# Optimization experiments

Measured on AMD Instinct MI355X. Metric: run time of the kernel, lower is better.

Reference implementation:

```python
import jax, jax.numpy as jnp
import numpy as np

B, T, C, H = 4, 2048, 768, 12
D = C // H  # head dim = 64

def setup_inputs() -> dict:
    key = jax.random.key(0)
    k1, k2, k3 = jax.random.split(key, 3)
    x = jax.random.normal(k1, (B, T, C), dtype=jnp.float32)
    W_attn = jax.random.normal(k2, (C, 3 * C), dtype=jnp.float32) * 0.02
    b_attn = jnp.zeros((3 * C,), dtype=jnp.float32)
    W_proj = jax.random.normal(k3, (C, C), dtype=jnp.float32) * 0.02
    b_proj = jnp.zeros((C,), dtype=jnp.float32)
    return {"x": x, "W_attn": W_attn, "b_attn": b_attn, "W_proj": W_proj, "b_proj": b_proj}

def reference(x, W_attn, b_attn, W_proj, b_proj):
    Bx, Tx, Cx = x.shape
    qkv = x @ W_attn + b_attn                      # [B,T,3C]
    q, k, v = jnp.split(qkv, 3, axis=2)
    q = q.reshape(Bx, Tx, H, D).swapaxes(1, 2)     # [B,H,T,D]
    k = k.reshape(Bx, Tx, H, D).swapaxes(1, 2)
    v = v.reshape(Bx, Tx, H, D).swapaxes(1, 2)
    att = jnp.einsum('bhqd,bhkd->bhqk', q, k) / jnp.sqrt(jnp.float32(D))
    mask = jnp.tril(jnp.ones((Tx, Tx), dtype=bool))
    att = jnp.where(mask, att, -jnp.inf)
    att = jax.nn.softmax(att, axis=-1)
    y = jnp.einsum('bhqk,bhkd->bhqd', att, v)      # [B,H,T,D]
    y = y.swapaxes(1, 2).reshape(Bx, Tx, Cx)
    return y @ W_proj + b_proj
```

## Files before the change

### kernel.cpp

```cpp
#include <hip/hip_runtime.h>
#include <hip/hip_bf16.h>

#define BATCH 4
#define TSEQ  2048
#define CDIM  768
#define HNUM  12
#define DHEAD 64
#define NQKV  (3*CDIM)
#define BTOT  (BATCH*TSEQ)
#define BH    (BATCH*HNUM)

typedef unsigned short u16;
typedef __attribute__((ext_vector_type(8))) __bf16 bf16x8;
typedef __attribute__((ext_vector_type(4))) float f32x4;

#define MFMA16(a,b,c) __builtin_amdgcn_mfma_f32_16x16x32_bf16((a),(b),(c),0,0,0)

__device__ __forceinline__ u16 f2b(float f) {
    union { float f; unsigned u; } v; v.f = f;
    unsigned u = v.u;
    unsigned r = (u + 0x7fffu + ((u >> 16) & 1u)) >> 16;
    return (u16)r;
}

__device__ __forceinline__ unsigned cvtpk(float lo, float hi) {
    unsigned r;
    asm("v_cvt_pk_bf16_f32 %0, %1, %2" : "=v"(r) : "v"(lo), "v"(hi));
    return r;
}

__device__ __forceinline__ float fexp2(float x) {
    float r;
    asm("v_exp_f32 %0, %1" : "=v"(r) : "v"(x));
    return r;
}

__device__ __forceinline__ void gload_lds(const void* g, void* l) {
    __builtin_amdgcn_global_load_lds(
        (const __attribute__((address_space(1))) void*)g,
        (__attribute__((address_space(3))) void*)l, 16, 0, 0);
}

#define CAST_BLKS (BTOT * CDIM / 4 / 256)
#define TA_BLKS   ((NQKV / 32) * (CDIM / 32))
#define TP_BLKS   ((CDIM / 32) * (CDIM / 32))
__global__ __launch_bounds__(256) void prep(
        const float* __restrict__ x, u16* __restrict__ xb,
        const float* __restrict__ Wa, const float* __restrict__ Wp,
        u16* __restrict__ WaT, u16* __restrict__ WpT) {
    __shared__ float tile[32][33];
    const int bx = blockIdx.x, tid = threadIdx.x;
    if (bx < CAST_BLKS) {
        int i = bx * 256 + tid;
        float4 a = reinterpret_cast<const float4*>(x)[i];
        ushort4 o;
        o.x = f2b(a.x); o.y = f2b(a.y); o.z = f2b(a.z); o.w = f2b(a.w);
        reinterpret_cast<ushort4*>(xb)[i] = o;
        return;
    }
    int bz = bx - CAST_BLKS;
    const float* in; u16* out; int Cc;
    int nxa = NQKV / 32;
    int cx, ry;
    if (bz < TA_BLKS) { in = Wa; out = WaT; Cc = NQKV; cx = bz % nxa; ry = bz / nxa; }
    else { bz -= TA_BLKS; in = Wp; out = WpT; Cc = CDIM; cx = bz % (CDIM/32); ry = bz / (CDIM/32); }
    int c0 = cx * 32, r0 = ry * 32;
    int tx = tid & 31, ty = tid >> 5;
    #pragma unroll
    for (int i = 0; i < 32; i += 8)
        tile[ty + i][tx] = in[(size_t)(r0 + ty + i) * Cc + c0 + tx];
    __syncthreads();
    #pragma unroll
    for (int i = 0; i < 32; i += 8)
        out[(size_t)(c0 + ty + i) * CDIM + r0 + tx] = f2b(tile[tx][ty + i]);
}

template<int NX>
__global__ __launch_bounds__(512) void gemm_qkv(
        const u16* __restrict__ A, const u16* __restrict__ Bt,
        const float* __restrict__ bias,
        u16* __restrict__ qb, u16* __restrict__ kb, u16* __restrict__ vtb,
        int K) {
    __shared__ u16 sA[2][256 * 32];
    __shared__ u16 sB[2][128 * 32];
    const int tid = threadIdx.x;
    const int lane = tid & 63;
    const int w = tid >> 6;
    const int wr = w >> 1, wc = w & 1;
    const int g = lane >> 4, lq = lane & 15;
    const int cpx = gridDim.x >> 3;
    const int wg = ((int)blockIdx.x & 7) * cpx + ((int)blockIdx.x >> 3);
    const int bx = wg % NX, by = wg / NX;
    const int m0 = by * 256, n0 = bx * 128;

    f32x4 acc[4][4] = {};

    auto stage = [&](int buf, int kt) {
        #pragma unroll
        for (int i = 0; i < 2; ++i) {
            int c = i * 512 + tid;
            int r = c >> 2, s = c & 3;
            int l = s ^ ((r >> 1) & 3);
            gload_lds(A + (size_t)(m0 + r) * K + kt * 32 + l * 8, &sA[buf][c * 8]);
        }
        {
            int c = tid;
            int r = c >> 2, s = c & 3;
            int l = s ^ ((r >> 1) & 3);
            gload_lds(Bt + (size_t)(n0 + r) * K + kt * 32 + l * 8, &sB[buf][c * 8]);
        }
    };

    const int KT = K / 32;
    stage(0, 0);
    __syncthreads();
    for (int kt = 0; kt < KT; ++kt) {
        if (kt + 1 < KT) stage((kt + 1) & 1, kt + 1);
        const u16* cA = sA[kt & 1];
        const u16* cB = sB[kt & 1];
        bf16x8 af[4], bfr[4];
        #pragma unroll
        for (int m = 0; m < 4; ++m) {
            int r = wr * 64 + m * 16 + lq;
            af[m] = *(const bf16x8*)&cA[r * 32 + ((g ^ ((r >> 1) & 3)) << 3)];
        }
        #pragma unroll
        for (int n = 0; n < 4; ++n) {
            int r = wc * 64 + n * 16 + lq;
            bfr[n] = *(const bf16x8*)&cB[r * 32 + ((g ^ ((r >> 1) & 3)) << 3)];
        }
        #pragma unroll
        for (int m = 0; m < 4; ++m)
            #pragma unroll
            for (int n = 0; n < 4; ++n)
                acc[m][n] = MFMA16(bfr[n], af[m], acc[m][n]);
        __syncthreads();
    }

    const int which = n0 / CDIM;
    #pragma unroll
    for (int m = 0; m < 4; ++m) {
        const int rg = m0 + wr * 64 + m * 16 + lq;
        const int b = rg >> 11, t = rg & (TSEQ - 1);
        #pragma unroll
        for (int n = 0; n < 4; ++n) {
            const int cg = n0 + wc * 64 + n * 16 + (g << 2);
            const int c  = cg - which * CDIM;
            const int h  = c >> 6, d = c & 63;
            const size_t bh = (size_t)(b * HNUM + h);
            const float4 bv = *(const float4*)&bias[cg];
            const float v0 = acc[m][n][0] + bv.x;
            const float v1 = acc[m][n][1] + bv.y;
            const float v2 = acc[m][n][2] + bv.z;
            const float v3 = acc[m][n][3] + bv.w;
            if (which == 0) {
                const float s = 0.1803368801111243f;
                ushort4 pv;
                pv.x = f2b(v0 * s); pv.y = f2b(v1 * s);
                pv.z = f2b(v2 * s); pv.w = f2b(v3 * s);
                *(ushort4*)&qb[(bh * TSEQ + t) * DHEAD + d] = pv;
            } else if (which == 1) {
                ushort4 pv;
                pv.x = f2b(v0); pv.y = f2b(v1); pv.z = f2b(v2); pv.w = f2b(v3);
                *(ushort4*)&kb[(bh * TSEQ + t) * DHEAD + d] = pv;
            } else {
                vtb[(bh * DHEAD + d + 0) * TSEQ + t] = f2b(v0);
                vtb[(bh * DHEAD + d + 1) * TSEQ + t] = f2b(v1);
                vtb[(bh * DHEAD + d + 2) * TSEQ + t] = f2b(v2);
                vtb[(bh * DHEAD + d + 3) * TSEQ + t] = f2b(v3);
            }
        }
    }
}

template<int NX>
__global__ __launch_bounds__(256) void gemm_out(
        const u16* __restrict__ A, const u16* __restrict__ Bt,
        const float* __restrict__ bias, float* __restrict__ outf, int K) {
    __shared__ u16 sA[2][64 * 32];
    __shared__ u16 sB[2][128 * 32];
    const int tid = threadIdx.x;
    const int lane = tid & 63;
    const int w = tid >> 6;
    const int wr = w >> 1, wc = w & 1;
    const int g = lane >> 4, lq = lane & 15;
    const int cpx = gridDim.x >> 3;
    const int wg = ((int)blockIdx.x & 7) * cpx + ((int)blockIdx.x >> 3);
    const int bx = wg % NX, by = wg / NX;
    const int m0 = by * 64, n0 = bx * 128;

    f32x4 acc[2][4] = {};

    auto stage = [&](int buf, int kt) {
        {
            int c = tid;
            int r = c >> 2, s = c & 3;
            int l = s ^ ((r >> 1) & 3);
            gload_lds(A + (size_t)(m0 + r) * K + kt * 32 + l * 8, &sA[buf][c * 8]);
        }
        #pragma unroll
        for (int i = 0; i < 2; ++i) {
            int c = i * 256 + tid;
            int r = c >> 2, s = c & 3;
            int l = s ^ ((r >> 1) & 3);
            gload_lds(Bt + (size_t)(n0 + r) * K + kt * 32 + l * 8, &sB[buf][c * 8]);
        }
    };

    const int KT = K / 32;
    stage(0, 0);
    __syncthreads();
    for (int kt = 0; kt < KT; ++kt) {
        if (kt + 1 < KT) stage((kt + 1) & 1, kt + 1);
        const u16* cA = sA[kt & 1];
        const u16* cB = sB[kt & 1];
        bf16x8 af[2], bfr[4];
        #pragma unroll
        for (int m = 0; m < 2; ++m) {
            int r = wr * 32 + m * 16 + lq;
            af[m] = *(const bf16x8*)&cA[r * 32 + ((g ^ ((r >> 1) & 3)) << 3)];
        }
        #pragma unroll
        for (int n = 0; n < 4; ++n) {
            int r = wc * 64 + n * 16 + lq;
            bfr[n] = *(const bf16x8*)&cB[r * 32 + ((g ^ ((r >> 1) & 3)) << 3)];
        }
        #pragma unroll
        for (int m = 0; m < 2; ++m)
            #pragma unroll
            for (int n = 0; n < 4; ++n)
                acc[m][n] = MFMA16(bfr[n], af[m], acc[m][n]);
        __syncthreads();
    }

    #pragma unroll
    for (int m = 0; m < 2; ++m) {
        const int rg = m0 + wr * 32 + m * 16 + lq;
        #pragma unroll
        for (int n = 0; n < 4; ++n) {
            const int cg = n0 + wc * 64 + n * 16 + (g << 2);
            const float4 bv = *(const float4*)&bias[cg];
            float4 ov;
            ov.x = acc[m][n][0] + bv.x;
            ov.y = acc[m][n][1] + bv.y;
            ov.z = acc[m][n][2] + bv.z;
            ov.w = acc[m][n][3] + bv.w;
            *(float4*)&outf[(size_t)rg * CDIM + cg] = ov;
        }
    }
}

__global__ __launch_bounds__(256, 5) void attn_fwd(
        const u16* __restrict__ qb, const u16* __restrict__ kb,
        const u16* __restrict__ vtb, u16* __restrict__ yb) {
    __shared__ u16 sK[2][64 * 64];
    __shared__ u16 sVt[2][64 * 64];
    const int qt = 31 - (int)(blockIdx.x / BH);
    const int bh = blockIdx.x % BH;
    const int b = bh / HNUM, h = bh % HNUM;
    const int tid = threadIdx.x, lane = tid & 63, w = tid >> 6;
    const int g = lane >> 4, lq = lane & 15;
    const int qlo = qt * 64 + w * 16;
    const u16* qbase = qb  + (size_t)bh * TSEQ * DHEAD;
    const u16* kbase = kb  + (size_t)bh * TSEQ * DHEAD;
    const u16* vbase = vtb + (size_t)bh * DHEAD * TSEQ;

    bf16x8 qf[2];
    #pragma unroll
    for (int ks = 0; ks < 2; ++ks)
        qf[ks] = *(const bf16x8*)&qbase[(size_t)(qlo + lq) * DHEAD + ks * 32 + g * 8];

    union { unsigned u[4]; bf16x8 v; } ones;
    #pragma unroll
    for (int i = 0; i < 4; ++i) ones.u[i] = 0x3f803f80u;

    f32x4 o[4] = {};
    f32x4 ls = {};
    float mx = -__builtin_inff();

    auto STAGE = [&](int buf, int kt) {
        const int k0 = kt << 6;
        #pragma unroll
        for (int i = 0; i < 2; ++i) {
            int chunk = i * 256 + tid;
            int srow = chunk >> 3;
            int cb = ((chunk & 7) << 4) ^ ((srow & 7) << 4);
            gload_lds(kbase + (size_t)(k0 + srow) * DHEAD + (cb >> 1), &sK[buf][chunk * 8]);
            gload_lds(vbase + (size_t)srow * TSEQ + k0 + (cb >> 1),    &sVt[buf][chunk * 8]);
        }
    };

    const int nk = qt + 1;
    STAGE(0, 0);
    __syncthreads();
    for (int kt = 0; kt < nk; ++kt) {
        const int k0 = kt << 6;
        if (kt + 1 < nk) STAGE((kt + 1) & 1, kt + 1);
        const u16* cK = sK[kt & 1];
        const u16* cV = sVt[kt & 1];
        f32x4 s[4];
        #pragma unroll
        for (int n = 0; n < 4; ++n) s[n] = f32x4{0.f, 0.f, 0.f, 0.f};
        __builtin_amdgcn_s_setprio(1);
        #pragma unroll
        for (int n = 0; n < 4; ++n) {
            #pragma unroll
            for (int ks = 0; ks < 2; ++ks) {
                int r = n * 16 + lq;
                int lb = (r * 128 + (ks * 32 + g * 8) * 2) ^ ((r & 7) << 4);
                bf16x8 kf = *(const bf16x8*)((const char*)cK + lb);
                s[n] = MFMA16(kf, qf[ks], s[n]);
            }
        }
        __builtin_amdgcn_s_setprio(0);
        if (k0 + 63 > qlo) {
            const int qa = qlo + lq;
            #pragma unroll
            for (int n = 0; n < 4; ++n)
                #pragma unroll
                for (int j = 0; j < 4; ++j)
                    if (k0 + n * 16 + g * 4 + j > qa) s[n][j] = -__builtin_inff();
        }
        float t0 = fmaxf(fmaxf(s[0][0], s[0][1]), fmaxf(s[0][2], s[0][3]));
        float t1 = fmaxf(fmaxf(s[1][0], s[1][1]), fmaxf(s[1][2], s[1][3]));
        float t2 = fmaxf(fmaxf(s[2][0], s[2][1]), fmaxf(s[2][2], s[2][3]));
        float t3 = fmaxf(fmaxf(s[3][0], s[3][1]), fmaxf(s[3][2], s[3][3]));
        float tmax = fmaxf(fmaxf(t0, t1), fmaxf(t2, t3));
        tmax = fmaxf(tmax, __shfl_xor(tmax, 16));
        tmax = fmaxf(tmax, __shfl_xor(tmax, 32));
        if (__any(tmax > mx + 8.0f)) {
            float mnew = fmaxf(mx, tmax);
            float sc = fexp2(mx - mnew);
            mx = mnew;
            #pragma unroll
            for (int j = 0; j < 4; ++j) {
                float scj = __shfl(sc, (lane & 48) | ((g << 2) + j));
                ls[j] *= scj;
                #pragma unroll
                for (int n = 0; n < 4; ++n) o[n][j] *= scj;
            }
        }
        #pragma unroll
        for (int n = 0; n < 4; ++n)
            #pragma unroll
            for (int j = 0; j < 4; ++j)
                s[n][j] = fexp2(s[n][j] - mx);
        unsigned apk[4], bpk[4];
        #pragma unroll
        for (int n = 0; n < 4; ++n) {
            apk[n] = cvtpk(s[n][0], s[n][1]);
            bpk[n] = cvtpk(s[n][2], s[n][3]);
        }
        const int s0l = lq + ((lane & 16) << 1);
        const bool hi = (lane & 32) != 0;
        #pragma unroll
        for (int ks = 0; ks < 2; ++ks) {
            unsigned A0  = (unsigned)__shfl((int)apk[2 * ks],     s0l);
            unsigned B0  = (unsigned)__shfl((int)bpk[2 * ks],     s0l);
            unsigned A1  = (unsigned)__shfl((int)apk[2 * ks + 1], s0l);
            unsigned B1  = (unsigned)__shfl((int)bpk[2 * ks + 1], s0l);
            unsigned A0h = (unsigned)__shfl((int)apk[2 * ks],     s0l + 16);
            unsigned B0h = (unsigned)__shfl((int)bpk[2 * ks],     s0l + 16);
            unsigned A1h = (unsigned)__shfl((int)apk[2 * ks + 1], s0l + 16);
            unsigned B1h = (unsigned)__shfl((int)bpk[2 * ks + 1], s0l + 16);
            union { unsigned u[4]; bf16x8 v; } pa;
            pa.u[0] = hi ? A1  : A0;
            pa.u[1] = hi ? B1  : B0;
            pa.u[2] = hi ? A1h : A0h;
            pa.u[3] = hi ? B1h : B0h;
            __builtin_amdgcn_s_setprio(1);
            #pragma unroll
            for (int n = 0; n < 4; ++n) {
                int d = n * 16 + lq;
                int lb = (d * 128 + (ks * 32 + g * 8) * 2) ^ ((d & 7) << 4);
                bf16x8 vf = *(const bf16x8*)((const char*)cV + lb);
                o[n] = MFMA16(pa.v, vf, o[n]);
            }
            ls = MFMA16(pa.v, ones.v, ls);
            __builtin_amdgcn_s_setprio(0);
        }
        __syncthreads();
    }

    #pragma unroll
    for (int j = 0; j < 4; ++j) {
        float inv = 1.f / ls[j];
        const int t = qlo + g * 4 + j;
        #pragma unroll
        for (int n = 0; n < 4; ++n) {
            const int c = h * DHEAD + n * 16 + lq;
            yb[((size_t)b * TSEQ + t) * CDIM + c] = f2b(o[n][j] * inv);
        }
    }
}

extern "C" void kernel_launch(void* const* d_in, const int* in_sizes, int n_in,
                              void* d_out, int out_size, void* d_ws, size_t ws_size,
                              hipStream_t stream) {
    const float* x      = (const float*)d_in[0];
    const float* W_attn = (const float*)d_in[1];
    const float* b_attn = (const float*)d_in[2];
    const float* W_proj = (const float*)d_in[3];
    const float* b_proj = (const float*)d_in[4];
    float* out = (float*)d_out;

    u16* ws = (u16*)d_ws;
    u16* xb     = ws;
    u16* yb     = xb;
    u16* WattnT = xb     + (size_t)BTOT * CDIM;
    u16* WprojT = WattnT + (size_t)NQKV * CDIM;
    u16* qb     = WprojT + (size_t)CDIM * CDIM;
    u16* kb     = qb     + (size_t)BH * TSEQ * DHEAD;
    u16* vtb    = kb     + (size_t)BH * TSEQ * DHEAD;

    prep<<<dim3(CAST_BLKS + TA_BLKS + TP_BLKS), 256, 0, stream>>>(
        x, xb, W_attn, W_proj, WattnT, WprojT);

    gemm_qkv<NQKV / 128><<<dim3((NQKV / 128) * (BTOT / 256)), 512, 0, stream>>>(
        xb, WattnT, b_attn, qb, kb, vtb, CDIM);

    attn_fwd<<<dim3((TSEQ / 64) * BH), 256, 0, stream>>>(qb, kb, vtb, yb);

    gemm_out<CDIM / 128><<<dim3((CDIM / 128) * (BTOT / 64)), 256, 0, stream>>>(
        yb, WprojT, b_proj, out, CDIM);
}
```

Measured before the change: 140.9 us.

## Triple-buffer QKV GEMM with BK=64 and interleaved load/MFMA phases

Changes the QKV projection GEMM from a double-buffered K-step of 32 to a triple-buffered K-step of 64. Prefetch now runs two tiles ahead, with an explicit vmcnt wait in place of __syncthreads. Each iteration is split into four sub-phases that interleave global-to-LDS staging, LDS fragment loads, and MFMA bursts, with setprio raised around the MFMAs. The goal is to hide memory latency and cut loop overhead per K element. The costs are much more LDS per block (about 144KB), which can limit occupancy, plus many extra barriers.

```diff
diff --git a/kernel.cpp b/kernel.cpp
--- a/kernel.cpp
+++ b/kernel.cpp
@@ -81,8 +81,8 @@
         const float* __restrict__ bias,
         u16* __restrict__ qb, u16* __restrict__ kb, u16* __restrict__ vtb,
         int K) {
-    __shared__ u16 sA[2][256 * 32];
-    __shared__ u16 sB[2][128 * 32];
+    __shared__ u16 sA[3][256 * 64];
+    __shared__ u16 sB[3][128 * 64];
     const int tid = threadIdx.x;
     const int lane = tid & 63;
     const int w = tid >> 6;
@@ -95,46 +95,90 @@
 
     f32x4 acc[4][4] = {};
 
-    auto stage = [&](int buf, int kt) {
-        #pragma unroll
-        for (int i = 0; i < 2; ++i) {
-            int c = i * 512 + tid;
-            int r = c >> 2, s = c & 3;
-            int l = s ^ ((r >> 1) & 3);
-            gload_lds(A + (size_t)(m0 + r) * K + kt * 32 + l * 8, &sA[buf][c * 8]);
-        }
-        {
-            int c = tid;
-            int r = c >> 2, s = c & 3;
-            int l = s ^ ((r >> 1) & 3);
-            gload_lds(Bt + (size_t)(n0 + r) * K + kt * 32 + l * 8, &sB[buf][c * 8]);
-        }
+    auto STA = [&](int buf, int t, int i) {
+        int c = i * 512 + tid;
+        int r = c >> 3, ks = (c >> 2) & 1, s = c & 3;
+        int l = s ^ ((r >> 1) & 3);
+        gload_lds(A + (size_t)(m0 + r) * K + t * 64 + ks * 32 + l * 8,
+                  &sA[buf][c * 8]);
     };
-
-    const int KT = K / 32;
-    stage(0, 0);
-    __syncthreads();
-    for (int kt = 0; kt < KT; ++kt) {
-        if (kt + 1 < KT) stage((kt + 1) & 1, kt + 1);
-        const u16* cA = sA[kt & 1];
-        const u16* cB = sB[kt & 1];
-        bf16x8 af[4], bfr[4];
+    auto STB = [&](int buf, int t, int i) {
+        int c = i * 512 + tid;
+        int r = c >> 3, ks = (c >> 2) & 1, s = c & 3;
+        int l = s ^ ((r >> 1) & 3);
+        gload_lds(Bt + (size_t)(n0 + r) * K + t * 64 + ks * 32 + l * 8,
+                  &sB[buf][c * 8]);
+    };
+    auto STALL6 = [&](int buf, int t) {
+        STA(buf, t, 0); STA(buf, t, 1); STA(buf, t, 2); STA(buf, t, 3);
+        STB(buf, t, 0); STB(buf, t, 1);
+    };
+
+    const int KT = K / 64;
+    STALL6(0, 0);
+    STALL6(1, 1);
+    for (int t = 0; t < KT; ++t) {
+        if (t + 1 < KT) asm volatile("s_waitcnt vmcnt(6)" ::: "memory");
+        else            asm volatile("s_waitcnt vmcnt(0)" ::: "memory");
+        __builtin_amdgcn_s_barrier();
+        const u16* cA = sA[t % 3];
+        const u16* cB = sB[t % 3];
+        const int nb = (t + 2) % 3;
+        const bool pre = (t + 2) < KT;
+
+        bf16x8 af[4], bf0, bf1;
+        #define LDA(m, ks) (*(const bf16x8*)&cA[(wr*64 + (m)*16 + lq) * 64 + (ks)*32 \
+                              + ((g ^ (((wr*64 + (m)*16 + lq) >> 1) & 3)) << 3)])
+        #define LDB(n, ks) (*(const bf16x8*)&cB[(wc*64 + (n)*16 + lq) * 64 + (ks)*32 \
+                              + ((g ^ (((wc*64 + (n)*16 + lq) >> 1) & 3)) << 3)])
+
+        if (pre) { STA(nb, t + 2, 0); STA(nb, t + 2, 1); }
+        af[0] = LDA(0, 0); af[1] = LDA(1, 0); af[2] = LDA(2, 0); af[3] = LDA(3, 0);
+        bf0 = LDB(0, 0); bf1 = LDB(1, 0);
+        __builtin_amdgcn_s_barrier();
+        __builtin_amdgcn_s_setprio(1);
         #pragma unroll
         for (int m = 0; m < 4; ++m) {
-            int r = wr * 64 + m * 16 + lq;
-            af[m] = *(const bf16x8*)&cA[r * 32 + ((g ^ ((r >> 1) & 3)) << 3)];
-        }
-        #pragma unroll
-        for (int n = 0; n < 4; ++n) {
-            int r = wc * 64 + n * 16 + lq;
-            bfr[n] = *(const bf16x8*)&cB[r * 32 + ((g ^ ((r >> 1) & 3)) << 3)];
-        }
-        #pragma unroll
-        for (int m = 0; m < 4; ++m)
-            #pragma unroll
-            for (int n = 0; n < 4; ++n)
-                acc[m][n] = MFMA16(bfr[n], af[m], acc[m][n]);
-        __syncthreads();
+            acc[m][0] = MFMA16(bf0, af[m], acc[m][0]);
+            acc[m][1] = MFMA16(bf1, af[m], acc[m][1]);
+        }
+        __builtin_amdgcn_s_setprio(0);
+        __builtin_amdgcn_s_barrier();
+        if (pre) { STA(nb, t + 2, 2); STA(nb, t + 2, 3); }
+        bf0 = LDB(2, 0); bf1 = LDB(3, 0);
+        __builtin_amdgcn_s_barrier();
+        __builtin_amdgcn_s_setprio(1);
+        #pragma unroll
+        for (int m = 0; m < 4; ++m) {
+            acc[m][2] = MFMA16(bf0, af[m], acc[m][2]);
+            acc[m][3] = MFMA16(bf1, af[m], acc[m][3]);
+        }
+        __builtin_amdgcn_s_setprio(0);
+        __builtin_amdgcn_s_barrier();
+        if (pre) { STB(nb, t + 2, 0); STB(nb, t + 2, 1); }
+        af[0] = LDA(0, 1); af[1] = LDA(1, 1); af[2] = LDA(2, 1); af[3] = LDA(3, 1);
+        bf0 = LDB(0, 1); bf1 = LDB(1, 1);
+        __builtin_amdgcn_s_barrier();
+        __builtin_amdgcn_s_setprio(1);
+        #pragma unroll
+        for (int m = 0; m < 4; ++m) {
+            acc[m][0] = MFMA16(bf0, af[m], acc[m][0]);
+            acc[m][1] = MFMA16(bf1, af[m], acc[m][1]);
+        }
+        __builtin_amdgcn_s_setprio(0);
+        __builtin_amdgcn_s_barrier();
+        bf0 = LDB(2, 1); bf1 = LDB(3, 1);
+        __builtin_amdgcn_s_barrier();
+        __builtin_amdgcn_s_setprio(1);
+        #pragma unroll
+        for (int m = 0; m < 4; ++m) {
+            acc[m][2] = MFMA16(bf0, af[m], acc[m][2]);
+            acc[m][3] = MFMA16(bf1, af[m], acc[m][3]);
+        }
+        __builtin_amdgcn_s_setprio(0);
+        __builtin_amdgcn_s_barrier();
+        #undef LDA
+        #undef LDB
     }
 
     const int which = n0 / CDIM;
```

Result: slower. 176.6 us (+25.4%).
